# Kernel optimization log

Hardware: AMD Instinct MI355X
Metric: run time of the kernel (lower is better)

The kernel has to match this reference:

```python
import jax, jax.numpy as jnp
import numpy as np

L, T, D = 3, 65536, 256


def setup_inputs() -> dict:
    key = jax.random.key(0)
    ks = jax.random.split(key, 10)
    stdv = 1.0 / np.sqrt(D)
    u = lambda k, shape: jax.random.uniform(k, shape, jnp.float32, -stdv, stdv)
    return {
        "story": jax.random.normal(ks[0], (T, D), jnp.float32),
        "question": jax.random.normal(ks[1], (D,), jnp.float32),
        "Wz_f": u(ks[2], (L, D, D)),
        "bz_f": u(ks[3], (L, D)),
        "Wh_f": u(ks[4], (L, 2 * D, D)),
        "bh_f": u(ks[5], (L, D)),
        "Wz_b": u(ks[6], (L, D, D)),
        "bz_b": u(ks[7], (L, D)),
        "Wh_b": u(ks[8], (L, 2 * D, D)),
        "bh_b": u(ks[9], (L, D)),
    }


def _qrn_dir(x, q, Wz, bz, Wh, bh):
    """One QRN layer in one direction. x, q: [T, D]. Returns h states [T, D]."""
    z = jax.nn.sigmoid((x * q) @ Wz + bz)                      # [T, D]
    h_tilde = jnp.tanh(jnp.concatenate([x, q], axis=-1) @ Wh + bh)  # [T, D]
    a = 1.0 - z            # multiplicative factor on h_prev
    b = z * h_tilde        # additive term
    # linear recurrence h_t = a_t * h_{t-1} + b_t, h_0 = 0 -> associative scan
    def comb(c1, c2):
        a1, b1 = c1
        a2, b2 = c2
        return a1 * a2, a2 * b1 + b2
    _, h = jax.lax.associative_scan(comb, (a, b), axis=0)
    return h  # h[t] = hidden state after statement t


def reference(story, question, Wz_f, bz_f, Wh_f, bh_f, Wz_b, bz_b, Wh_b, bh_b):
    q = jnp.broadcast_to(question, story.shape)  # layer-0 question per step
    for layer in range(L):
        h_fwd = _qrn_dir(story, q, Wz_f[layer], bz_f[layer], Wh_f[layer], bh_f[layer])
        # backward direction: reversed story with correspondingly reversed questions
        h_bwd_rev = _qrn_dir(story[::-1], q[::-1], Wz_b[layer], bz_b[layer],
                             Wh_b[layer], bh_b[layer])
        if layer < L - 1:
            # q_{t}^{k+1} = h_fwd_t + h_bwd_t (aligned back to forward order)
            q = h_fwd + h_bwd_rev[::-1]
    return h_fwd[-1]  # final forward hidden state of last layer, [D]
```

## Files before the change

kernel.cpp:

```cpp
#include <hip/hip_runtime.h>
#include <hip/hip_bf16.h>
#include <math.h>

#define D    256
#define BT   128
#define GN   128
#define NSEG 32

typedef unsigned short u16;
typedef unsigned int   u32;
typedef __attribute__((ext_vector_type(8))) short short8;
typedef __attribute__((ext_vector_type(4))) float floatx4;

__device__ __forceinline__ float b2f(u16 v) {
    union { unsigned u; float f; } x; x.u = ((unsigned)v) << 16; return x.f;
}
__device__ __forceinline__ u16 f2b(float f) {
    union { unsigned u; float f; } x; x.f = f;
    unsigned lsb = (x.u >> 16) & 1;
    x.u += 0x7fffu + lsb;
    return (u16)(x.u >> 16);
}
__device__ __forceinline__ float sigm(float x) {
    return __builtin_amdgcn_rcpf(1.0f + __expf(-x));
}
__device__ __forceinline__ float tanhfast(float x) {
    return 1.0f - 2.0f * __builtin_amdgcn_rcpf(__expf(2.0f * x) + 1.0f);
}
__device__ __forceinline__ void async16(const u16* g, u16* l) {
    __builtin_amdgcn_global_load_lds(
        (const __attribute__((address_space(1))) unsigned int*)g,
        (__attribute__((address_space(3))) unsigned int*)l, 16, 0, 0);
}

__global__ __launch_bounds__(256) void wtrans_kernel(
    const float* __restrict__ Wz_f, const float* __restrict__ Wh_f,
    const float* __restrict__ Wz_b, const float* __restrict__ Wh_b,
    u16* __restrict__ wt)
{
    int id = blockIdx.x * 256 + threadIdx.x;
    int combo = id / (3 * 65536);
    int rem   = id % (3 * 65536);
    int m = rem >> 16;
    int e = rem & 65535;
    int k = e >> 8, n = e & 255;
    int l   = combo < 3 ? combo : combo - 3;
    int dir = combo < 3 ? 0 : 1;
    float v;
    if (m == 0) {
        const float* Wz = dir ? Wz_b : Wz_f;
        v = Wz[((size_t)l * D + k) * D + n];
    } else {
        const float* Wh = dir ? Wh_b : Wh_f;
        int kk = (m == 2) ? (k + D) : k;
        v = Wh[((size_t)l * 2 * D + kk) * D + n];
    }
    wt[(size_t)combo * 3 * 65536 + (size_t)m * 65536 + (size_t)n * D + k] = f2b(v);
}

__global__ __launch_bounds__(256) void prep0_kernel(
    const float* __restrict__ story, const float* __restrict__ question,
    u16* __restrict__ xb, u16* __restrict__ q, u16* __restrict__ xq)
{
    long id = (long)blockIdx.x * 256 + threadIdx.x;
    long row = id >> 5;
    int  d0  = (int)(id & 31) * 8;
    const float* xp = story + row * D + d0;
    float4 xa = *(const float4*)xp;
    float4 xc = *(const float4*)(xp + 4);
    float xv[8] = {xa.x, xa.y, xa.z, xa.w, xc.x, xc.y, xc.z, xc.w};
    short8 xs, qs, xqs;
    #pragma unroll
    for (int i = 0; i < 8; ++i) {
        u16 qb = f2b(question[d0 + i]);
        xs[i]  = (short)f2b(xv[i]);
        qs[i]  = (short)qb;
        xqs[i] = (short)f2b(xv[i] * b2f(qb));
    }
    long o = id * 8;
    *(short8*)(xb + o) = xs;
    *(short8*)(q  + o) = qs;
    *(short8*)(xq + o) = xqs;
}

struct StageS {
    u16 ax [BT * 32]; u16 aq [BT * 32]; u16 axq[BT * 32];
    u16 bz_[GN * 32]; u16 bx_[GN * 32]; u16 bq_[GN * 32];
};
struct EpiP { float segA[NSEG][GN]; float segB[NSEG][GN]; };
union __align__(16) SharedP { StageS st; EpiP ep; };

__device__ __forceinline__ void gemm_body(
    SharedP& sh, int tid, int c, int n0,
    const u16* xbg, const u16* qg, const u16* xqg, const u16* wt,
    const float* bz, const float* bh,
    float* aggA, float* aggB, u32* abg, int FWD)
{
    const int t0   = c * BT;
    const int lane = tid & 63, w = tid >> 6;
    const int wr = w & 1, wc = w >> 1;
    const int lr   = lane & 15, quad = lane >> 4;

    const int swA   = (quad ^ ((lr >> 1) & 3)) * 8;
    const int offA0 = (wr * 64 + lr) * 32 + swA;
    const int offB0 = (wc * 32 + lr) * 32 + swA;

    floatx4 accz[4][2], acch[4][2];
    #pragma unroll
    for (int rt = 0; rt < 4; ++rt)
        #pragma unroll
        for (int ct = 0; ct < 2; ++ct) {
            accz[rt][ct] = (floatx4){0.f,0.f,0.f,0.f};
            acch[rt][ct] = (floatx4){0.f,0.f,0.f,0.f};
        }

    const int lb = (tid & ~63) * 8;

    const int arow = tid >> 2;
    const int agg_ = (tid & 3) ^ ((arow >> 1) & 3);
    const size_t goA = (size_t)(t0 + arow) * D + agg_ * 8;
    const size_t goB = (size_t)(n0 + arow) * D + agg_ * 8;
    const u16* pax  = xbg + goA;
    const u16* paq  = qg  + goA;
    const u16* paxq = xqg + goA;
    const u16* pbz  = wt + goB;
    const u16* pbx  = wt + 65536  + goB;
    const u16* pbq  = wt + 131072 + goB;

    #pragma unroll
    for (int k0 = 0; k0 < D; k0 += 32) {
        async16(pax  + k0, sh.st.ax  + lb);
        async16(paq  + k0, sh.st.aq  + lb);
        async16(paxq + k0, sh.st.axq + lb);
        async16(pbz  + k0, sh.st.bz_ + lb);
        async16(pbx  + k0, sh.st.bx_ + lb);
        async16(pbq  + k0, sh.st.bq_ + lb);
        __syncthreads();

        short8 vz[2], vx[2], vq[2];
        #pragma unroll
        for (int ct = 0; ct < 2; ++ct) {
            vz[ct] = *(const short8*)(sh.st.bz_ + offB0 + ct * 512);
            vx[ct] = *(const short8*)(sh.st.bx_ + offB0 + ct * 512);
            vq[ct] = *(const short8*)(sh.st.bq_ + offB0 + ct * 512);
        }
        #pragma unroll
        for (int rt = 0; rt < 4; ++rt) {
            short8 fxq = *(const short8*)(sh.st.axq + offA0 + rt * 512);
            short8 fx  = *(const short8*)(sh.st.ax  + offA0 + rt * 512);
            short8 fq  = *(const short8*)(sh.st.aq  + offA0 + rt * 512);
            #pragma unroll
            for (int ct = 0; ct < 2; ++ct) {
                accz[rt][ct] = __builtin_amdgcn_mfma_f32_16x16x32_bf16(fxq, vz[ct], accz[rt][ct], 0, 0, 0);
                acch[rt][ct] = __builtin_amdgcn_mfma_f32_16x16x32_bf16(fx , vx[ct], acch[rt][ct], 0, 0, 0);
                acch[rt][ct] = __builtin_amdgcn_mfma_f32_16x16x32_bf16(fq , vq[ct], acch[rt][ct], 0, 0, 0);
            }
        }
        __syncthreads();
    }

    float bzn[2], bhn[2];
    #pragma unroll
    for (int ct = 0; ct < 2; ++ct) {
        int n = n0 + wc * 32 + ct * 16 + lr;
        bzn[ct] = bz[n]; bhn[ct] = bh[n];
    }
    float av[4][2][4], bvv[4][2][4];
    #pragma unroll
    for (int rt = 0; rt < 4; ++rt) {
        #pragma unroll
        for (int ct = 0; ct < 2; ++ct) {
            #pragma unroll
            for (int r = 0; r < 4; ++r) {
                float z  = sigm(accz[rt][ct][r] + bzn[ct]);
                float ht = tanhfast(acch[rt][ct][r] + bhn[ct]);
                av[rt][ct][r]  = 1.0f - z;
                bvv[rt][ct][r] = z * ht;
            }
            float A = 1.f, B = 0.f;
            if (FWD) {
                #pragma unroll
                for (int r = 0; r < 4; ++r) { A = av[rt][ct][r] * A; B = fmaf(av[rt][ct][r], B, bvv[rt][ct][r]); }
            } else {
                #pragma unroll
                for (int r = 3; r >= 0; --r) { A = av[rt][ct][r] * A; B = fmaf(av[rt][ct][r], B, bvv[rt][ct][r]); }
            }
            int seg = wr * 16 + rt * 4 + quad;
            int col = wc * 32 + ct * 16 + lr;
            sh.ep.segA[seg][col] = A;
            sh.ep.segB[seg][col] = B;
        }
    }
    __syncthreads();

    if (tid < GN) {
        float A = 1.f, B = 0.f;
        if (FWD) {
            #pragma unroll
            for (int sg = 0; sg < NSEG; ++sg) {
                float a = sh.ep.segA[sg][tid], b = sh.ep.segB[sg][tid];
                sh.ep.segA[sg][tid] = A; sh.ep.segB[sg][tid] = B;
                A = a * A; B = fmaf(a, B, b);
            }
        } else {
            #pragma unroll
            for (int sg = NSEG - 1; sg >= 0; --sg) {
                float a = sh.ep.segA[sg][tid], b = sh.ep.segB[sg][tid];
                sh.ep.segA[sg][tid] = A; sh.ep.segB[sg][tid] = B;
                A = a * A; B = fmaf(a, B, b);
            }
        }
        aggA[(size_t)c * D + n0 + tid] = A;
        aggB[(size_t)c * D + n0 + tid] = B;
    }

    if (abg) {
        __syncthreads();
        #pragma unroll
        for (int rt = 0; rt < 4; ++rt) {
            #pragma unroll
            for (int ct = 0; ct < 2; ++ct) {
                int seg = wr * 16 + rt * 4 + quad;
                int col = wc * 32 + ct * 16 + lr;
                float Pa = sh.ep.segA[seg][col];
                float Pb = sh.ep.segB[seg][col];
                size_t base = (size_t)(t0 + wr * 64 + rt * 16 + quad * 4) * D + n0 + col;
                if (FWD) {
                    #pragma unroll
                    for (int r = 0; r < 4; ++r) {
                        Pa = av[rt][ct][r] * Pa;
                        Pb = fmaf(av[rt][ct][r], Pb, bvv[rt][ct][r]);
                        abg[base + (size_t)r * D] = (u32)f2b(Pa) | ((u32)f2b(Pb) << 16);
                    }
                } else {
                    #pragma unroll
                    for (int r = 3; r >= 0; --r) {
                        Pa = av[rt][ct][r] * Pa;
                        Pb = fmaf(av[rt][ct][r], Pb, bvv[rt][ct][r]);
                        abg[base + (size_t)r * D] = (u32)f2b(Pa) | ((u32)f2b(Pb) << 16);
                    }
                }
            }
        }
    }
}

template<int FWD, int ABOUT>
__global__ __launch_bounds__(512, 4) void qrn_g5(
    const u16* __restrict__ xbg, const u16* __restrict__ qg,
    const u16* __restrict__ xqg, const u16* __restrict__ wt,
    const float* __restrict__ bz, const float* __restrict__ bh,
    float* __restrict__ aggA, float* __restrict__ aggB,
    u32* __restrict__ abg)
{
    __shared__ SharedP sh;
    const int tid  = threadIdx.x;
    const int bid  = (int)blockIdx.x;
    const int gidx = (bid & 7) * 128 + (bid >> 3);
    gemm_body(sh, tid, gidx >> 1, (gidx & 1) * GN,
              xbg, qg, xqg, wt, bz, bh, aggA, aggB, ABOUT ? abg : nullptr, FWD);
}

__global__ __launch_bounds__(512, 4) void qrn_gboth(
    const u16* __restrict__ xbg, const u16* __restrict__ qg,
    const u16* __restrict__ xqg,
    const u16* __restrict__ wtF, const u16* __restrict__ wtB,
    const float* __restrict__ bzf, const float* __restrict__ bhf,
    const float* __restrict__ bzb, const float* __restrict__ bhb,
    float* __restrict__ aggAf, float* __restrict__ aggBf,
    float* __restrict__ aggAb, float* __restrict__ aggBb,
    u32* __restrict__ abf, u32* __restrict__ abb)
{
    __shared__ SharedP sh;
    const int tid  = threadIdx.x;
    const int half = (int)blockIdx.x >> 10;
    const int bid  = (int)blockIdx.x & 1023;
    const int gidx = (bid & 7) * 128 + (bid >> 3);
    gemm_body(sh, tid, gidx >> 1, (gidx & 1) * GN,
              xbg, qg, xqg,
              half ? wtB : wtF,
              half ? bzb : bzf, half ? bhb : bhf,
              half ? aggAb : aggAf, half ? aggBb : aggBf,
              half ? abb : abf, half ? 0 : 1);
}

__global__ __launch_bounds__(256) void replay2_fb(
    const u32* __restrict__ abf, const u32* __restrict__ abb,
    const float* __restrict__ hinif, const float* __restrict__ hinib,
    const u16* __restrict__ xb, u16* __restrict__ qout, u16* __restrict__ xq,
    int total8)
{
    for (int id = (int)blockIdx.x * 256 + (int)threadIdx.x; id < total8;
         id += (int)gridDim.x * 256) {
        int t  = id >> 5;
        int n0 = (id & 31) * 8;
        int c  = t >> 7;
        size_t o  = (size_t)t * D + n0;
        size_t hc = (size_t)c * D + n0;
        uint4 f0 = *(const uint4*)(abf + o);
        uint4 f1 = *(const uint4*)(abf + o + 4);
        uint4 g0 = *(const uint4*)(abb + o);
        uint4 g1 = *(const uint4*)(abb + o + 4);
        float4 hf0 = *(const float4*)(hinif + hc);
        float4 hf1 = *(const float4*)(hinif + hc + 4);
        float4 hb0 = *(const float4*)(hinib + hc);
        float4 hb1 = *(const float4*)(hinib + hc + 4);
        short8 xv = *(const short8*)(xb + o);
        u32 fa[8] = {f0.x, f0.y, f0.z, f0.w, f1.x, f1.y, f1.z, f1.w};
        u32 ga[8] = {g0.x, g0.y, g0.z, g0.w, g1.x, g1.y, g1.z, g1.w};
        float hfv[8] = {hf0.x, hf0.y, hf0.z, hf0.w, hf1.x, hf1.y, hf1.z, hf1.w};
        float hbv[8] = {hb0.x, hb0.y, hb0.z, hb0.w, hb1.x, hb1.y, hb1.z, hb1.w};
        short8 qs, xqs;
        #pragma unroll
        for (int i = 0; i < 8; ++i) {
            float hF = fmaf(b2f((u16)(fa[i] & 0xffff)), hfv[i], b2f((u16)(fa[i] >> 16)));
            float hB = fmaf(b2f((u16)(ga[i] & 0xffff)), hbv[i], b2f((u16)(ga[i] >> 16)));
            u16 qb = f2b(hF + hB);
            qs[i]  = (short)qb;
            xqs[i] = (short)f2b(b2f((u16)xv[i]) * b2f(qb));
        }
        *(short8*)(qout + o) = qs;
        *(short8*)(xq + o)   = xqs;
    }
}

__global__ __launch_bounds__(256) void replay2_f(
    const u32* __restrict__ abg, const float* __restrict__ hini,
    u16* __restrict__ qout, int total8)
{
    for (int id = (int)blockIdx.x * 256 + (int)threadIdx.x; id < total8;
         id += (int)gridDim.x * 256) {
        int t  = id >> 5;
        int n0 = (id & 31) * 8;
        int c  = t >> 7;
        size_t o  = (size_t)t * D + n0;
        size_t hc = (size_t)c * D + n0;
        uint4 f0 = *(const uint4*)(abg + o);
        uint4 f1 = *(const uint4*)(abg + o + 4);
        float4 hf0 = *(const float4*)(hini + hc);
        float4 hf1 = *(const float4*)(hini + hc + 4);
        u32 fa[8] = {f0.x, f0.y, f0.z, f0.w, f1.x, f1.y, f1.z, f1.w};
        float hfv[8] = {hf0.x, hf0.y, hf0.z, hf0.w, hf1.x, hf1.y, hf1.z, hf1.w};
        short8 qs;
        #pragma unroll
        for (int i = 0; i < 8; ++i) {
            float hF = fmaf(b2f((u16)(fa[i] & 0xffff)), hfv[i], b2f((u16)(fa[i] >> 16)));
            qs[i] = (short)f2b(hF);
        }
        *(short8*)(qout + o) = qs;
    }
}

__global__ __launch_bounds__(256) void replay2_b(
    const u32* __restrict__ abg, const float* __restrict__ hini,
    const u16* __restrict__ xb, u16* __restrict__ qout, u16* __restrict__ xq,
    int total8)
{
    for (int id = (int)blockIdx.x * 256 + (int)threadIdx.x; id < total8;
         id += (int)gridDim.x * 256) {
        int t  = id >> 5;
        int n0 = (id & 31) * 8;
        int c  = t >> 7;
        size_t o  = (size_t)t * D + n0;
        size_t hc = (size_t)c * D + n0;
        uint4 g0 = *(const uint4*)(abg + o);
        uint4 g1 = *(const uint4*)(abg + o + 4);
        float4 hb0 = *(const float4*)(hini + hc);
        float4 hb1 = *(const float4*)(hini + hc + 4);
        short8 qold = *(const short8*)(qout + o);
        short8 xv   = *(const short8*)(xb + o);
        u32 ga[8] = {g0.x, g0.y, g0.z, g0.w, g1.x, g1.y, g1.z, g1.w};
        float hbv[8] = {hb0.x, hb0.y, hb0.z, hb0.w, hb1.x, hb1.y, hb1.z, hb1.w};
        short8 qs, xqs;
        #pragma unroll
        for (int i = 0; i < 8; ++i) {
            float hB = fmaf(b2f((u16)(ga[i] & 0xffff)), hbv[i], b2f((u16)(ga[i] >> 16)));
            float qn = b2f((u16)qold[i]) + hB;
            u16 qb = f2b(qn);
            qs[i]  = (short)qb;
            xqs[i] = (short)f2b(b2f((u16)xv[i]) * b2f(qb));
        }
        *(short8*)(qout + o) = qs;
        *(short8*)(xq + o)   = xqs;
    }
}

__device__ __forceinline__ void scan_body(
    const float* aggA, const float* aggB, float* hinit, float* out_final,
    int fwd, int nch, int n, int tid)
{
    __shared__ float sA[256], sB[256];
    const int per = nch >> 8;
    float lA[4], lB[4];
    float A = 1.f, B = 0.f;
    for (int j = 0; j < per; ++j) {
        int pidx = tid * per + j;
        int c = fwd ? pidx : (nch - 1 - pidx);
        float a = aggA[(size_t)c * D + n];
        float b = aggB[(size_t)c * D + n];
        lA[j] = a; lB[j] = b;
        A = a * A;
        B = fmaf(a, B, b);
    }
    sA[tid] = A; sB[tid] = B;
    __syncthreads();
    for (int off = 1; off < 256; off <<= 1) {
        float pA = 1.f, pB = 0.f;
        if (tid >= off) { pA = sA[tid - off]; pB = sB[tid - off]; }
        __syncthreads();
        if (tid >= off) {
            float cA = sA[tid], cB = sB[tid];
            sA[tid] = pA * cA;
            sB[tid] = fmaf(cA, pB, cB);
        }
        __syncthreads();
    }
    float eB = (tid > 0) ? sB[tid - 1] : 0.f;
    for (int j = 0; j < per; ++j) {
        int pidx = tid * per + j;
        int c = fwd ? pidx : (nch - 1 - pidx);
        hinit[(size_t)c * D + n] = eB;
        eB = fmaf(lA[j], eB, lB[j]);
    }
    if (out_final != nullptr && tid == 0) out_final[n] = sB[255];
}

__global__ __launch_bounds__(256) void scan_p2_kernel(
    const float* __restrict__ aggA, const float* __restrict__ aggB,
    float* __restrict__ hinit, float* __restrict__ out_final, int fwd, int nch)
{
    scan_body(aggA, aggB, hinit, out_final, fwd, nch, blockIdx.x, threadIdx.x);
}

__global__ __launch_bounds__(256) void scan_dual_kernel(
    const float* __restrict__ aggAf, const float* __restrict__ aggBf, float* __restrict__ hf,
    const float* __restrict__ aggAb, const float* __restrict__ aggBb, float* __restrict__ hb,
    int nch)
{
    int b = blockIdx.x;
    int fwd = (b < D) ? 1 : 0;
    int n = fwd ? b : (b - D);
    scan_body(fwd ? aggAf : aggAb, fwd ? aggBf : aggBb,
              fwd ? hf : hb, nullptr, fwd, nch, n, threadIdx.x);
}

extern "C" void kernel_launch(void* const* d_in, const int* in_sizes, int n_in,
                              void* d_out, int out_size, void* d_ws, size_t ws_size,
                              hipStream_t stream) {
    const float* story    = (const float*)d_in[0];
    const float* question = (const float*)d_in[1];
    const float* Wz_f = (const float*)d_in[2];
    const float* bz_f = (const float*)d_in[3];
    const float* Wh_f = (const float*)d_in[4];
    const float* bh_f = (const float*)d_in[5];
    const float* Wz_b = (const float*)d_in[6];
    const float* bz_b = (const float*)d_in[7];
    const float* Wh_b = (const float*)d_in[8];
    const float* bh_b = (const float*)d_in[9];

    const int T    = in_sizes[0] / D;
    const int NCH  = T / BT;
    const size_t TD = (size_t)T * D;
    const size_t WTE = 5 * 3 * 65536;
    const int total8 = T * 32;

    const size_t needF = 3 * TD * 2 + WTE * 2 + 2 * TD * 4
                       + (size_t)4 * NCH * D * 4 + 4096;
    const bool planF = ws_size >= needF;

    dim3 blk(256);
    dim3 gblk(512);
    dim3 gGrid((unsigned)(NCH * 2));
    dim3 g2Grid((unsigned)(NCH * 4));
    dim3 rGrid(2048);
    dim3 pGrid((unsigned)(TD / 8 / 256));

    if (planF) {
        u16* xb = (u16*)d_ws;
        u16* q  = xb + TD;
        u16* xq = q  + TD;
        u16* wt = xq + TD;
        u32* abf = (u32*)(wt + WTE);
        u32* abb = abf + TD;
        float* aggAf = (float*)(abb + TD);
        float* aggBf = aggAf + (size_t)NCH * D;
        float* aggAb = aggBf + (size_t)NCH * D;
        float* aggBb = aggAb + (size_t)NCH * D;
        float* hinif = aggBf;
        float* hinib = aggBb;

        wtrans_kernel<<<dim3(5 * 3 * 65536 / 256), blk, 0, stream>>>(
            Wz_f, Wh_f, Wz_b, Wh_b, wt);
        prep0_kernel<<<pGrid, blk, 0, stream>>>(story, question, xb, q, xq);

        for (int l = 0; l < 3; ++l) {
            const u16*   wtf = wt + (size_t)l * 3 * 65536;
            const float* bzf = bz_f + (size_t)l * D;
            const float* bhf = bh_f + (size_t)l * D;

            if (l == 2) {
                qrn_g5<1,0><<<gGrid, gblk, 0, stream>>>(
                    xb, q, xq, wtf, bzf, bhf, aggAf, aggBf, nullptr);
                scan_p2_kernel<<<dim3(D), blk, 0, stream>>>(
                    aggAf, aggBf, hinif, (float*)d_out, 1, NCH);
                break;
            }
            const u16*   wtb = wt + (size_t)(3 + l) * 3 * 65536;
            const float* bzb = bz_b + (size_t)l * D;
            const float* bhb = bh_b + (size_t)l * D;

            qrn_gboth<<<g2Grid, gblk, 0, stream>>>(
                xb, q, xq, wtf, wtb, bzf, bhf, bzb, bhb,
                aggAf, aggBf, aggAb, aggBb, abf, abb);
            scan_dual_kernel<<<dim3(2 * D), blk, 0, stream>>>(
                aggAf, aggBf, hinif, aggAb, aggBb, hinib, NCH);
            replay2_fb<<<rGrid, blk, 0, stream>>>(
                abf, abb, hinif, hinib, xb, q, xq, total8);
        }
    } else {
        u16* xb = (u16*)d_ws;
        u16* qA = xb + TD;
        u16* qB = qA + TD;
        u16* xq = qB + TD;
        u16* wt = xq + TD;
        u32*   ab   = (u32*)(wt + WTE);
        float* aggA = (float*)(ab + TD);
        float* aggB = aggA + (size_t)NCH * D;
        float* hini = aggB;

        wtrans_kernel<<<dim3(5 * 3 * 65536 / 256), blk, 0, stream>>>(
            Wz_f, Wh_f, Wz_b, Wh_b, wt);
        prep0_kernel<<<pGrid, blk, 0, stream>>>(story, question, xb, qA, xq);

        const u16* qcur  = qA;
        u16*       qnext = qB;

        for (int l = 0; l < 3; ++l) {
            const u16*   wtf = wt + (size_t)l * 3 * 65536;
            const float* bzf = bz_f + (size_t)l * D;
            const float* bhf = bh_f + (size_t)l * D;

            if (l == 2) {
                qrn_g5<1,0><<<gGrid, gblk, 0, stream>>>(
                    xb, qcur, xq, wtf, bzf, bhf, aggA, aggB, nullptr);
                scan_p2_kernel<<<dim3(D), blk, 0, stream>>>(
                    aggA, aggB, hini, (float*)d_out, 1, NCH);
                break;
            }
            const u16*   wtb = wt + (size_t)(3 + l) * 3 * 65536;
            const float* bzb = bz_b + (size_t)l * D;
            const float* bhb = bh_b + (size_t)l * D;

            qrn_g5<1,1><<<gGrid, gblk, 0, stream>>>(
                xb, qcur, xq, wtf, bzf, bhf, aggA, aggB, ab);
            scan_p2_kernel<<<dim3(D), blk, 0, stream>>>(aggA, aggB, hini, nullptr, 1, NCH);
            replay2_f<<<rGrid, blk, 0, stream>>>(ab, hini, qnext, total8);

            qrn_g5<0,1><<<gGrid, gblk, 0, stream>>>(
                xb, qcur, xq, wtb, bzb, bhb, aggA, aggB, ab);
            scan_p2_kernel<<<dim3(D), blk, 0, stream>>>(aggA, aggB, hini, nullptr, 0, NCH);
            replay2_b<<<rGrid, blk, 0, stream>>>(ab, hini, xb, qnext, xq, total8);

            const u16* ts = qcur; qcur = qnext; qnext = (u16*)ts;
        }
    }
}
```

Baseline: 438.3 us.

## Double-buffer LDS staging in GEMM loop and relax launch bounds

Splits the shared-memory staging area into two buffers. Each k-step now issues the async global-to-LDS copies for the next K slice before running the MFMAs on the current slice, and the per-iteration barrier before compute is removed. This hides global load latency behind matrix work. It doubles staging LDS to about 96KB per block, which cuts how many 512-thread blocks fit on a CU. Launch bounds drop from 4 to 2 blocks per SM, so the compiler may use more registers, at the cost of fewer resident waves for latency hiding.

Result: slower. 523.5 us (+19.4%).

```diff
diff --git a/kernel.cpp b/kernel.cpp
--- a/kernel.cpp
+++ b/kernel.cpp
@@ -87,8 +87,9 @@
     u16 ax [BT * 32]; u16 aq [BT * 32]; u16 axq[BT * 32];
     u16 bz_[GN * 32]; u16 bx_[GN * 32]; u16 bq_[GN * 32];
 };
+struct StageD { StageS buf[2]; };
 struct EpiP { float segA[NSEG][GN]; float segB[NSEG][GN]; };
-union __align__(16) SharedP { StageS st; EpiP ep; };
+union __align__(16) SharedP { StageD st; EpiP ep; };
 
 __device__ __forceinline__ void gemm_body(
     SharedP& sh, int tid, int c, int n0,
@@ -127,28 +128,35 @@
     const u16* pbx  = wt + 65536  + goB;
     const u16* pbq  = wt + 131072 + goB;
 
+    auto stage = [&](StageS& b, int k0) {
+        async16(pax  + k0, b.ax  + lb);
+        async16(paq  + k0, b.aq  + lb);
+        async16(paxq + k0, b.axq + lb);
+        async16(pbz  + k0, b.bz_ + lb);
+        async16(pbx  + k0, b.bx_ + lb);
+        async16(pbq  + k0, b.bq_ + lb);
+    };
+
+    stage(sh.st.buf[0], 0);
+    __syncthreads();
+
     #pragma unroll
-    for (int k0 = 0; k0 < D; k0 += 32) {
-        async16(pax  + k0, sh.st.ax  + lb);
-        async16(paq  + k0, sh.st.aq  + lb);
-        async16(paxq + k0, sh.st.axq + lb);
-        async16(pbz  + k0, sh.st.bz_ + lb);
-        async16(pbx  + k0, sh.st.bx_ + lb);
-        async16(pbq  + k0, sh.st.bq_ + lb);
-        __syncthreads();
-
+    for (int kk = 0; kk < 8; ++kk) {
+        if (kk < 7) stage(sh.st.buf[(kk + 1) & 1], (kk + 1) * 32);
+
+        const StageS& S = sh.st.buf[kk & 1];
         short8 vz[2], vx[2], vq[2];
         #pragma unroll
         for (int ct = 0; ct < 2; ++ct) {
-            vz[ct] = *(const short8*)(sh.st.bz_ + offB0 + ct * 512);
-            vx[ct] = *(const short8*)(sh.st.bx_ + offB0 + ct * 512);
-            vq[ct] = *(const short8*)(sh.st.bq_ + offB0 + ct * 512);
+            vz[ct] = *(const short8*)(S.bz_ + offB0 + ct * 512);
+            vx[ct] = *(const short8*)(S.bx_ + offB0 + ct * 512);
+            vq[ct] = *(const short8*)(S.bq_ + offB0 + ct * 512);
         }
         #pragma unroll
         for (int rt = 0; rt < 4; ++rt) {
-            short8 fxq = *(const short8*)(sh.st.axq + offA0 + rt * 512);
-            short8 fx  = *(const short8*)(sh.st.ax  + offA0 + rt * 512);
-            short8 fq  = *(const short8*)(sh.st.aq  + offA0 + rt * 512);
+            short8 fxq = *(const short8*)(S.axq + offA0 + rt * 512);
+            short8 fx  = *(const short8*)(S.ax  + offA0 + rt * 512);
+            short8 fq  = *(const short8*)(S.aq  + offA0 + rt * 512);
             #pragma unroll
             for (int ct = 0; ct < 2; ++ct) {
                 accz[rt][ct] = __builtin_amdgcn_mfma_f32_16x16x32_bf16(fxq, vz[ct], accz[rt][ct], 0, 0, 0);
@@ -246,7 +254,7 @@
 }
 
 template<int FWD, int ABOUT>
-__global__ __launch_bounds__(512, 4) void qrn_g5(
+__global__ __launch_bounds__(512, 2) void qrn_g5(
     const u16* __restrict__ xbg, const u16* __restrict__ qg,
     const u16* __restrict__ xqg, const u16* __restrict__ wt,
     const float* __restrict__ bz, const float* __restrict__ bh,
@@ -261,7 +269,7 @@
               xbg, qg, xqg, wt, bz, bh, aggA, aggB, ABOUT ? abg : nullptr, FWD);
 }
 
-__global__ __launch_bounds__(512, 4) void qrn_gboth(
+__global__ __launch_bounds__(512, 2) void qrn_gboth(
     const u16* __restrict__ xbg, const u16* __restrict__ qg,
     const u16* __restrict__ xqg,
     const u16* __restrict__ wtF, const u16* __restrict__ wtB,
```

## Fold constant layer-0 question into weights and bias, specialize layer-0 GEMM

Applied to the files above, without the earlier changes.

In layer 0 the question is the same for every step, so (x*q)@Wz becomes x@(diag(q)Wz) and q@Wh_q becomes a bias vector computed once by a new small kernel. A specialized layer-0 GEMM then loads only x and two weight tiles and issues two MFMAs per tile instead of three. prep0 no longer writes the broadcast q and x*q buffers, which cuts memory traffic. Rounding differs slightly because q is folded into the bf16 weights and the question term is now computed in fp32.

After: 439.4 us. No clear change (+0.2%).

```diff
diff --git a/kernel.cpp b/kernel.cpp
--- a/kernel.cpp
+++ b/kernel.cpp
@@ -34,6 +34,7 @@
 }
 
 __global__ __launch_bounds__(256) void wtrans_kernel(
+    const float* __restrict__ question,
     const float* __restrict__ Wz_f, const float* __restrict__ Wh_f,
     const float* __restrict__ Wz_b, const float* __restrict__ Wh_b,
     u16* __restrict__ wt)
@@ -50,6 +51,7 @@
     if (m == 0) {
         const float* Wz = dir ? Wz_b : Wz_f;
         v = Wz[((size_t)l * D + k) * D + n];
+        if (l == 0) v *= question[k];
     } else {
         const float* Wh = dir ? Wh_b : Wh_f;
         int kk = (m == 2) ? (k + D) : k;
@@ -58,106 +60,56 @@
     wt[(size_t)combo * 3 * 65536 + (size_t)m * 65536 + (size_t)n * D + k] = f2b(v);
 }
 
+__global__ __launch_bounds__(256) void bias0_kernel(
+    const float* __restrict__ question,
+    const float* __restrict__ Wh_f, const float* __restrict__ Wh_b,
+    const float* __restrict__ bh_f, const float* __restrict__ bh_b,
+    float* __restrict__ bh0f, float* __restrict__ bh0b)
+{
+    const float* Wh = blockIdx.x ? Wh_b : Wh_f;
+    const float* bh = blockIdx.x ? bh_b : bh_f;
+    float* out = blockIdx.x ? bh0b : bh0f;
+    int n = threadIdx.x;
+    float acc = bh[n];
+    for (int k = 0; k < D; ++k)
+        acc = fmaf(question[k], Wh[(size_t)(D + k) * D + n], acc);
+    out[n] = acc;
+}
+
 __global__ __launch_bounds__(256) void prep0_kernel(
-    const float* __restrict__ story, const float* __restrict__ question,
-    u16* __restrict__ xb, u16* __restrict__ q, u16* __restrict__ xq)
+    const float* __restrict__ story, u16* __restrict__ xb)
 {
     long id = (long)blockIdx.x * 256 + threadIdx.x;
-    long row = id >> 5;
-    int  d0  = (int)(id & 31) * 8;
-    const float* xp = story + row * D + d0;
+    const float* xp = story + id * 8;
     float4 xa = *(const float4*)xp;
     float4 xc = *(const float4*)(xp + 4);
     float xv[8] = {xa.x, xa.y, xa.z, xa.w, xc.x, xc.y, xc.z, xc.w};
-    short8 xs, qs, xqs;
+    short8 xs;
     #pragma unroll
-    for (int i = 0; i < 8; ++i) {
-        u16 qb = f2b(question[d0 + i]);
-        xs[i]  = (short)f2b(xv[i]);
-        qs[i]  = (short)qb;
-        xqs[i] = (short)f2b(xv[i] * b2f(qb));
-    }
-    long o = id * 8;
-    *(short8*)(xb + o) = xs;
-    *(short8*)(q  + o) = qs;
-    *(short8*)(xq + o) = xqs;
+    for (int i = 0; i < 8; ++i) xs[i] = (short)f2b(xv[i]);
+    *(short8*)(xb + id * 8) = xs;
 }
 
 struct StageS {
     u16 ax [BT * 32]; u16 aq [BT * 32]; u16 axq[BT * 32];
     u16 bz_[GN * 32]; u16 bx_[GN * 32]; u16 bq_[GN * 32];
 };
-struct EpiP { float segA[NSEG][GN]; float segB[NSEG][GN]; };
-union __align__(16) SharedP { StageS st; EpiP ep; };
-
-__device__ __forceinline__ void gemm_body(
-    SharedP& sh, int tid, int c, int n0,
-    const u16* xbg, const u16* qg, const u16* xqg, const u16* wt,
+struct Stage0 {
+    u16 ax [BT * 32]; u16 bz_[GN * 32]; u16 bx_[GN * 32];
+};
+struct EpiP  { float segA[NSEG][GN]; float segB[NSEG][GN]; };
+union __align__(16) SharedP  { StageS st; EpiP ep; };
+union __align__(16) SharedP0 { Stage0 st; EpiP ep; };
+
+__device__ __forceinline__ void gate_epilogue(
+    EpiP& ep, int tid, int t0, int n0,
+    floatx4 (&accz)[4][2], floatx4 (&acch)[4][2],
     const float* bz, const float* bh,
     float* aggA, float* aggB, u32* abg, int FWD)
 {
-    const int t0   = c * BT;
     const int lane = tid & 63, w = tid >> 6;
     const int wr = w & 1, wc = w >> 1;
-    const int lr   = lane & 15, quad = lane >> 4;
-
-    const int swA   = (quad ^ ((lr >> 1) & 3)) * 8;
-    const int offA0 = (wr * 64 + lr) * 32 + swA;
-    const int offB0 = (wc * 32 + lr) * 32 + swA;
-
-    floatx4 accz[4][2], acch[4][2];
-    #pragma unroll
-    for (int rt = 0; rt < 4; ++rt)
-        #pragma unroll
-        for (int ct = 0; ct < 2; ++ct) {
-            accz[rt][ct] = (floatx4){0.f,0.f,0.f,0.f};
-            acch[rt][ct] = (floatx4){0.f,0.f,0.f,0.f};
-        }
-
-    const int lb = (tid & ~63) * 8;
-
-    const int arow = tid >> 2;
-    const int agg_ = (tid & 3) ^ ((arow >> 1) & 3);
-    const size_t goA = (size_t)(t0 + arow) * D + agg_ * 8;
-    const size_t goB = (size_t)(n0 + arow) * D + agg_ * 8;
-    const u16* pax  = xbg + goA;
-    const u16* paq  = qg  + goA;
-    const u16* paxq = xqg + goA;
-    const u16* pbz  = wt + goB;
-    const u16* pbx  = wt + 65536  + goB;
-    const u16* pbq  = wt + 131072 + goB;
-
-    #pragma unroll
-    for (int k0 = 0; k0 < D; k0 += 32) {
-        async16(pax  + k0, sh.st.ax  + lb);
-        async16(paq  + k0, sh.st.aq  + lb);
-        async16(paxq + k0, sh.st.axq + lb);
-        async16(pbz  + k0, sh.st.bz_ + lb);
-        async16(pbx  + k0, sh.st.bx_ + lb);
-        async16(pbq  + k0, sh.st.bq_ + lb);
-        __syncthreads();
-
-        short8 vz[2], vx[2], vq[2];
-        #pragma unroll
-        for (int ct = 0; ct < 2; ++ct) {
-            vz[ct] = *(const short8*)(sh.st.bz_ + offB0 + ct * 512);
-            vx[ct] = *(const short8*)(sh.st.bx_ + offB0 + ct * 512);
-            vq[ct] = *(const short8*)(sh.st.bq_ + offB0 + ct * 512);
-        }
-        #pragma unroll
-        for (int rt = 0; rt < 4; ++rt) {
-            short8 fxq = *(const short8*)(sh.st.axq + offA0 + rt * 512);
-            short8 fx  = *(const short8*)(sh.st.ax  + offA0 + rt * 512);
-            short8 fq  = *(const short8*)(sh.st.aq  + offA0 + rt * 512);
-            #pragma unroll
-            for (int ct = 0; ct < 2; ++ct) {
-                accz[rt][ct] = __builtin_amdgcn_mfma_f32_16x16x32_bf16(fxq, vz[ct], accz[rt][ct], 0, 0, 0);
-                acch[rt][ct] = __builtin_amdgcn_mfma_f32_16x16x32_bf16(fx , vx[ct], acch[rt][ct], 0, 0, 0);
-                acch[rt][ct] = __builtin_amdgcn_mfma_f32_16x16x32_bf16(fq , vq[ct], acch[rt][ct], 0, 0, 0);
-            }
-        }
-        __syncthreads();
-    }
+    const int lr = lane & 15, quad = lane >> 4;
 
     float bzn[2], bhn[2];
     #pragma unroll
@@ -187,8 +139,8 @@
             }
             int seg = wr * 16 + rt * 4 + quad;
             int col = wc * 32 + ct * 16 + lr;
-            sh.ep.segA[seg][col] = A;
-            sh.ep.segB[seg][col] = B;
+            ep.segA[seg][col] = A;
+            ep.segB[seg][col] = B;
         }
     }
     __syncthreads();
@@ -198,18 +150,19 @@
         if (FWD) {
             #pragma unroll
             for (int sg = 0; sg < NSEG; ++sg) {
-                float a = sh.ep.segA[sg][tid], b = sh.ep.segB[sg][tid];
-                sh.ep.segA[sg][tid] = A; sh.ep.segB[sg][tid] = B;
+                float a = ep.segA[sg][tid], b = ep.segB[sg][tid];
+                ep.segA[sg][tid] = A; ep.segB[sg][tid] = B;
                 A = a * A; B = fmaf(a, B, b);
             }
         } else {
             #pragma unroll
             for (int sg = NSEG - 1; sg >= 0; --sg) {
-                float a = sh.ep.segA[sg][tid], b = sh.ep.segB[sg][tid];
-                sh.ep.segA[sg][tid] = A; sh.ep.segB[sg][tid] = B;
+                float a = ep.segA[sg][tid], b = ep.segB[sg][tid];
+                ep.segA[sg][tid] = A; ep.segB[sg][tid] = B;
                 A = a * A; B = fmaf(a, B, b);
             }
         }
+        int c = t0 / BT;
         aggA[(size_t)c * D + n0 + tid] = A;
         aggB[(size_t)c * D + n0 + tid] = B;
     }
@@ -222,8 +175,8 @@
             for (int ct = 0; ct < 2; ++ct) {
                 int seg = wr * 16 + rt * 4 + quad;
                 int col = wc * 32 + ct * 16 + lr;
-                float Pa = sh.ep.segA[seg][col];
-                float Pb = sh.ep.segB[seg][col];
+                float Pa = ep.segA[seg][col];
+                float Pb = ep.segB[seg][col];
                 size_t base = (size_t)(t0 + wr * 64 + rt * 16 + quad * 4) * D + n0 + col;
                 if (FWD) {
                     #pragma unroll
@@ -245,6 +198,139 @@
     }
 }
 
+__device__ __forceinline__ void gemm_body(
+    SharedP& sh, int tid, int c, int n0,
+    const u16* xbg, const u16* qg, const u16* xqg, const u16* wt,
+    const float* bz, const float* bh,
+    float* aggA, float* aggB, u32* abg, int FWD)
+{
+    const int t0   = c * BT;
+    const int lane = tid & 63, w = tid >> 6;
+    const int wr = w & 1, wc = w >> 1;
+    const int lr   = lane & 15, quad = lane >> 4;
+
+    const int swA   = (quad ^ ((lr >> 1) & 3)) * 8;
+    const int offA0 = (wr * 64 + lr) * 32 + swA;
+    const int offB0 = (wc * 32 + lr) * 32 + swA;
+
+    floatx4 accz[4][2], acch[4][2];
+    #pragma unroll
+    for (int rt = 0; rt < 4; ++rt)
+        #pragma unroll
+        for (int ct = 0; ct < 2; ++ct) {
+            accz[rt][ct] = (floatx4){0.f,0.f,0.f,0.f};
+            acch[rt][ct] = (floatx4){0.f,0.f,0.f,0.f};
+        }
+
+    const int lb = (tid & ~63) * 8;
+
+    const int arow = tid >> 2;
+    const int agg_ = (tid & 3) ^ ((arow >> 1) & 3);
+    const size_t goA = (size_t)(t0 + arow) * D + agg_ * 8;
+    const size_t goB = (size_t)(n0 + arow) * D + agg_ * 8;
+    const u16* pax  = xbg + goA;
+    const u16* paq  = qg  + goA;
+    const u16* paxq = xqg + goA;
+    const u16* pbz  = wt + goB;
+    const u16* pbx  = wt + 65536  + goB;
+    const u16* pbq  = wt + 131072 + goB;
+
+    #pragma unroll
+    for (int k0 = 0; k0 < D; k0 += 32) {
+        async16(pax  + k0, sh.st.ax  + lb);
+        async16(paq  + k0, sh.st.aq  + lb);
+        async16(paxq + k0, sh.st.axq + lb);
+        async16(pbz  + k0, sh.st.bz_ + lb);
+        async16(pbx  + k0, sh.st.bx_ + lb);
+        async16(pbq  + k0, sh.st.bq_ + lb);
+        __syncthreads();
+
+        short8 vz[2], vx[2], vq[2];
+        #pragma unroll
+        for (int ct = 0; ct < 2; ++ct) {
+            vz[ct] = *(const short8*)(sh.st.bz_ + offB0 + ct * 512);
+            vx[ct] = *(const short8*)(sh.st.bx_ + offB0 + ct * 512);
+            vq[ct] = *(const short8*)(sh.st.bq_ + offB0 + ct * 512);
+        }
+        #pragma unroll
+        for (int rt = 0; rt < 4; ++rt) {
+            short8 fxq = *(const short8*)(sh.st.axq + offA0 + rt * 512);
+            short8 fx  = *(const short8*)(sh.st.ax  + offA0 + rt * 512);
+            short8 fq  = *(const short8*)(sh.st.aq  + offA0 + rt * 512);
+            #pragma unroll
+            for (int ct = 0; ct < 2; ++ct) {
+                accz[rt][ct] = __builtin_amdgcn_mfma_f32_16x16x32_bf16(fxq, vz[ct], accz[rt][ct], 0, 0, 0);
+                acch[rt][ct] = __builtin_amdgcn_mfma_f32_16x16x32_bf16(fx , vx[ct], acch[rt][ct], 0, 0, 0);
+                acch[rt][ct] = __builtin_amdgcn_mfma_f32_16x16x32_bf16(fq , vq[ct], acch[rt][ct], 0, 0, 0);
+            }
+        }
+        __syncthreads();
+    }
+
+    gate_epilogue(sh.ep, tid, t0, n0, accz, acch, bz, bh, aggA, aggB, abg, FWD);
+}
+
+__device__ __forceinline__ void gemm0_body(
+    SharedP0& sh, int tid, int c, int n0,
+    const u16* xbg, const u16* wt,
+    const float* bz, const float* bh0,
+    float* aggA, float* aggB, u32* abg, int FWD)
+{
+    const int t0   = c * BT;
+    const int lane = tid & 63, w = tid >> 6;
+    const int wr = w & 1, wc = w >> 1;
+    const int lr   = lane & 15, quad = lane >> 4;
+
+    const int swA   = (quad ^ ((lr >> 1) & 3)) * 8;
+    const int offA0 = (wr * 64 + lr) * 32 + swA;
+    const int offB0 = (wc * 32 + lr) * 32 + swA;
+
+    floatx4 accz[4][2], acch[4][2];
+    #pragma unroll
+    for (int rt = 0; rt < 4; ++rt)
+        #pragma unroll
+        for (int ct = 0; ct < 2; ++ct) {
+            accz[rt][ct] = (floatx4){0.f,0.f,0.f,0.f};
+            acch[rt][ct] = (floatx4){0.f,0.f,0.f,0.f};
+        }
+
+    const int lb = (tid & ~63) * 8;
+    const int arow = tid >> 2;
+    const int agg_ = (tid & 3) ^ ((arow >> 1) & 3);
+    const size_t goA = (size_t)(t0 + arow) * D + agg_ * 8;
+    const size_t goB = (size_t)(n0 + arow) * D + agg_ * 8;
+    const u16* pax = xbg + goA;
+    const u16* pbz = wt + goB;
+    const u16* pbx = wt + 65536 + goB;
+
+    #pragma unroll
+    for (int k0 = 0; k0 < D; k0 += 32) {
+        async16(pax + k0, sh.st.ax  + lb);
+        async16(pbz + k0, sh.st.bz_ + lb);
+        async16(pbx + k0, sh.st.bx_ + lb);
+        __syncthreads();
+
+        short8 vz[2], vx[2];
+        #pragma unroll
+        for (int ct = 0; ct < 2; ++ct) {
+            vz[ct] = *(const short8*)(sh.st.bz_ + offB0 + ct * 512);
+            vx[ct] = *(const short8*)(sh.st.bx_ + offB0 + ct * 512);
+        }
+        #pragma unroll
+        for (int rt = 0; rt < 4; ++rt) {
+            short8 fx = *(const short8*)(sh.st.ax + offA0 + rt * 512);
+            #pragma unroll
+            for (int ct = 0; ct < 2; ++ct) {
+                accz[rt][ct] = __builtin_amdgcn_mfma_f32_16x16x32_bf16(fx, vz[ct], accz[rt][ct], 0, 0, 0);
+                acch[rt][ct] = __builtin_amdgcn_mfma_f32_16x16x32_bf16(fx, vx[ct], acch[rt][ct], 0, 0, 0);
+            }
+        }
+        __syncthreads();
+    }
+
+    gate_epilogue(sh.ep, tid, t0, n0, accz, acch, bz, bh0, aggA, aggB, abg, FWD);
+}
+
 template<int FWD, int ABOUT>
 __global__ __launch_bounds__(512, 4) void qrn_g5(
     const u16* __restrict__ xbg, const u16* __restrict__ qg,
@@ -282,6 +368,43 @@
               half ? bzb : bzf, half ? bhb : bhf,
               half ? aggAb : aggAf, half ? aggBb : aggBf,
               half ? abb : abf, half ? 0 : 1);
+}
+
+template<int FWD>
+__global__ __launch_bounds__(512, 4) void qrn_g0(
+    const u16* __restrict__ xbg, const u16* __restrict__ wt,
+    const float* __restrict__ bz, const float* __restrict__ bh0,
+    float* __restrict__ aggA, float* __restrict__ aggB,
+    u32* __restrict__ abg)
+{
+    __shared__ SharedP0 sh;
+    const int tid  = threadIdx.x;
+    const int bid  = (int)blockIdx.x;
+    const int gidx = (bid & 7) * 128 + (bid >> 3);
+    gemm0_body(sh, tid, gidx >> 1, (gidx & 1) * GN,
+               xbg, wt, bz, bh0, aggA, aggB, abg, FWD);
+}
+
+__global__ __launch_bounds__(512, 4) void qrn_g0both(
+    const u16* __restrict__ xbg,
+    const u16* __restrict__ wtF, const u16* __restrict__ wtB,
+    const float* __restrict__ bzf, const float* __restrict__ bh0f,
+    const float* __restrict__ bzb, const float* __restrict__ bh0b,
+    float* __restrict__ aggAf, float* __restrict__ aggBf,
+    float* __restrict__ aggAb, float* __restrict__ aggBb,
+    u32* __restrict__ abf, u32* __restrict__ abb)
+{
+    __shared__ SharedP0 sh;
+    const int tid  = threadIdx.x;
+    const int half = (int)blockIdx.x >> 10;
+    const int bid  = (int)blockIdx.x & 1023;
+    const int gidx = (bid & 7) * 128 + (bid >> 3);
+    gemm0_body(sh, tid, gidx >> 1, (gidx & 1) * GN,
+               xbg,
+               half ? wtB : wtF,
+               half ? bzb : bzf, half ? bh0b : bh0f,
+               half ? aggAb : aggAf, half ? aggBb : aggBf,
+               half ? abb : abf, half ? 0 : 1);
 }
 
 __global__ __launch_bounds__(256) void replay2_fb(
@@ -465,7 +588,7 @@
     const int total8 = T * 32;
 
     const size_t needF = 3 * TD * 2 + WTE * 2 + 2 * TD * 4
-                       + (size_t)4 * NCH * D * 4 + 4096;
+                       + (size_t)4 * NCH * D * 4 + 2 * D * 4 + 4096;
     const bool planF = ws_size >= needF;
 
     dim3 blk(256);
@@ -486,12 +609,16 @@
         float* aggBf = aggAf + (size_t)NCH * D;
         float* aggAb = aggBf + (size_t)NCH * D;
         float* aggBb = aggAb + (size_t)NCH * D;
+        float* bh0f  = aggBb + (size_t)NCH * D;
+        float* bh0b  = bh0f + D;
         float* hinif = aggBf;
         float* hinib = aggBb;
 
         wtrans_kernel<<<dim3(5 * 3 * 65536 / 256), blk, 0, stream>>>(
-            Wz_f, Wh_f, Wz_b, Wh_b, wt);
-        prep0_kernel<<<pGrid, blk, 0, stream>>>(story, question, xb, q, xq);
+            question, Wz_f, Wh_f, Wz_b, Wh_b, wt);
+        bias0_kernel<<<dim3(2), blk, 0, stream>>>(
+            question, Wh_f, Wh_b, bh_f, bh_b, bh0f, bh0b);
+        prep0_kernel<<<pGrid, blk, 0, stream>>>(story, xb);
 
         for (int l = 0; l < 3; ++l) {
             const u16*   wtf = wt + (size_t)l * 3 * 65536;
@@ -509,9 +636,15 @@
             const float* bzb = bz_b + (size_t)l * D;
             const float* bhb = bh_b + (size_t)l * D;
 
-            qrn_gboth<<<g2Grid, gblk, 0, stream>>>(
-                xb, q, xq, wtf, wtb, bzf, bhf, bzb, bhb,
-                aggAf, aggBf, aggAb, aggBb, abf, abb);
+            if (l == 0) {
+                qrn_g0both<<<g2Grid, gblk, 0, stream>>>(
+                    xb, wtf, wtb, bzf, bh0f, bzb, bh0b,
+                    aggAf, aggBf, aggAb, aggBb, abf, abb);
+            } else {
+                qrn_gboth<<<g2Grid, gblk, 0, stream>>>(
+                    xb, q, xq, wtf, wtb, bzf, bhf, bzb, bhb,
+                    aggAf, aggBf, aggAb, aggBb, abf, abb);
+            }
             scan_dual_kernel<<<dim3(2 * D), blk, 0, stream>>>(
                 aggAf, aggBf, hinif, aggAb, aggBb, hinib, NCH);
             replay2_fb<<<rGrid, blk, 0, stream>>>(
@@ -526,11 +659,15 @@
         u32*   ab   = (u32*)(wt + WTE);
         float* aggA = (float*)(ab + TD);
         float* aggB = aggA + (size_t)NCH * D;
+        float* bh0f = aggB + (size_t)NCH * D;
+        float* bh0b = bh0f + D;
         float* hini = aggB;
 
         wtrans_kernel<<<dim3(5 * 3 * 65536 / 256), blk, 0, stream>>>(
-            Wz_f, Wh_f, Wz_b, Wh_b, wt);
-        prep0_kernel<<<pGrid, blk, 0, stream>>>(story, question, xb, qA, xq);
+            question, Wz_f, Wh_f, Wz_b, Wh_b, wt);
+        bias0_kernel<<<dim3(2), blk, 0, stream>>>(
+            question, Wh_f, Wh_b, bh_f, bh_b, bh0f, bh0b);
+        prep0_kernel<<<pGrid, blk, 0, stream>>>(story, xb);
 
         const u16* qcur  = qA;
         u16*       qnext = qB;
@@ -551,16 +688,27 @@
             const float* bzb = bz_b + (size_t)l * D;
             const float* bhb = bh_b + (size_t)l * D;
 
-            qrn_g5<1,1><<<gGrid, gblk, 0, stream>>>(
-                xb, qcur, xq, wtf, bzf, bhf, aggA, aggB, ab);
-            scan_p2_kernel<<<dim3(D), blk, 0, stream>>>(aggA, aggB, hini, nullptr, 1, NCH);
-            replay2_f<<<rGrid, blk, 0, stream>>>(ab, hini, qnext, total8);
-
-            qrn_g5<0,1><<<gGrid, gblk, 0, stream>>>(
-                xb, qcur, xq, wtb, bzb, bhb, aggA, aggB, ab);
-            scan_p2_kernel<<<dim3(D), blk, 0, stream>>>(aggA, aggB, hini, nullptr, 0, NCH);
-            replay2_b<<<rGrid, blk, 0, stream>>>(ab, hini, xb, qnext, xq, total8);
-
+            if (l == 0) {
+                qrn_g0<1><<<gGrid, gblk, 0, stream>>>(
+                    xb, wtf, bzf, bh0f, aggA, aggB, ab);
+                scan_p2_kernel<<<dim3(D), blk, 0, stream>>>(aggA, aggB, hini, nullptr, 1, NCH);
+                replay2_f<<<rGrid, blk, 0, stream>>>(ab, hini, qnext, total8);
+
+                qrn_g0<0><<<gGrid, gblk, 0, stream>>>(
+                    xb, wtb, bzb, bh0b, aggA, aggB, ab);
+                scan_p2_kernel<<<dim3(D), blk, 0, stream>>>(aggA, aggB, hini, nullptr, 0, NCH);
+                replay2_b<<<rGrid, blk, 0, stream>>>(ab, hini, xb, qnext, xq, total8);
+            } else {
+                qrn_g5<1,1><<<gGrid, gblk, 0, stream>>>(
+                    xb, qcur, xq, wtf, bzf, bhf, aggA, aggB, ab);
+                scan_p2_kernel<<<dim3(D), blk, 0, stream>>>(aggA, aggB, hini, nullptr, 1, NCH);
+                replay2_f<<<rGrid, blk, 0, stream>>>(ab, hini, qnext, total8);
+
+                qrn_g5<0,1><<<gGrid, gblk, 0, stream>>>(
+                    xb, qcur, xq, wtb, bzb, bhb, aggA, aggB, ab);
+                scan_p2_kernel<<<dim3(D), blk, 0, stream>>>(aggA, aggB, hini, nullptr, 0, NCH);
+                replay2_b<<<rGrid, blk, 0, stream>>>(ab, hini, xb, qnext, xq, total8);
+            }
             const u16* ts = qcur; qcur = qnext; qnext = (u16*)ts;
         }
     }
```
